# Performance work log

Measured on AMD Instinct MI355X. Metric: run time of the kernel, lower is better.

The kernel has to match this reference:

```python
import jax, jax.numpy as jnp
import numpy as np

B, S, T, D = 4, 512, 512, 256


def setup_inputs() -> dict:
    key = jax.random.key(0)
    ks = jax.random.split(key, 10)
    scale = 1.0 / np.sqrt(D)
    return {
        "source": jax.random.normal(ks[0], (B, S, D), jnp.float32),
        "target": jax.random.normal(ks[1], (B, T, D), jnp.float32),
        "W_src": jax.random.uniform(ks[2], (D, D), jnp.float32, -scale, scale),
        "b_src": jax.random.uniform(ks[3], (D,), jnp.float32, -scale, scale),
        "W_tgt": jax.random.uniform(ks[4], (D, D), jnp.float32, -scale, scale),
        "b_tgt": jax.random.uniform(ks[5], (D,), jnp.float32, -scale, scale),
        "W_res": jax.random.uniform(ks[6], (D, 1), jnp.float32, -scale, scale),
        "b_res": jax.random.uniform(ks[7], (1,), jnp.float32, -scale, scale),
        "W_prob": jax.random.uniform(ks[8], (D, 2), jnp.float32, -scale, scale),
        "b_prob": jax.random.uniform(ks[9], (2,), jnp.float32, -scale, scale),
    }


def reference(source, target, W_src, b_src, W_tgt, b_tgt, W_res, b_res, W_prob, b_prob):
    # source: (B,S,D), target: (B,T,D)
    src_lin = jnp.einsum("bsd,de->bse", source, W_src) + b_src  # (B,S,D)
    tgt_lin = jnp.einsum("btd,de->bte", target, W_tgt) + b_tgt  # (B,T,D)
    # Bahdanau-style additive attention: (B,T,S,D) broadcast, tanh, D->1
    h = jnp.tanh(src_lin[:, None, :, :] + tgt_lin[:, :, None, :])  # (B,T,S,D)
    genP = jnp.einsum("btsd,d->bts", h, W_res[:, 0]) + b_res[0]     # (B,T,S)
    prob = jax.nn.softmax(jnp.einsum("btd,de->bte", target, W_prob) + b_prob, axis=-1)  # (B,T,2)
    return genP, prob
```

## Files before the change

kernel.cpp:

```cpp
#include <hip/hip_runtime.h>

#define B_ 4
#define S_ 512
#define T_ 512
#define D_ 256
#define NSRC (B_ * S_)
#define K2F 2.8853900817779268f

typedef __attribute__((ext_vector_type(8))) short short8;
typedef __attribute__((ext_vector_type(4))) float f32x4;
typedef __attribute__((ext_vector_type(2))) float f32x2;

__device__ __forceinline__ unsigned short f2bf(float f) {
    union { float f; unsigned u; } v; v.f = f;
    unsigned r = v.u + 0x7FFF + ((v.u >> 16) & 1);
    return (unsigned short)(r >> 16);
}

__global__ __launch_bounds__(256) void prep_kernel(
    const float* __restrict__ src, const float* __restrict__ tgt,
    const float* __restrict__ Wsrc, const float* __restrict__ Wtgt,
    const float* __restrict__ Wp, const float* __restrict__ bp,
    unsigned short* __restrict__ abf, unsigned short* __restrict__ wtb,
    float* __restrict__ out)
{
    __shared__ float tl[64 * 65];
    const int blk = blockIdx.x, tid = threadIdx.x;

    if (blk < 1024) {
        int i4 = blk * 256 + tid;
        const int half = NSRC * D_ / 4;
        const float4* in = (i4 < half) ? (const float4*)src : (const float4*)tgt;
        int j = (i4 < half) ? i4 : i4 - half;
        float4 v = in[j];
        ushort4 o;
        o.x = f2bf(v.x); o.y = f2bf(v.y); o.z = f2bf(v.z); o.w = f2bf(v.w);
        *(ushort4*)&abf[i4 * 4] = o;
    } else if (blk < 1056) {
        int wb = blk - 1024;
        int e = wb >> 4, ti = wb & 15, tr = ti >> 2, tc = ti & 3;
        int r0 = tr * 64, c0 = tc * 64;
        const float* W = e ? Wtgt : Wsrc;
        #pragma unroll
        for (int it = 0; it < 4; it++) {
            int rr = (tid >> 4) + it * 16;
            int cc = (tid & 15) * 4;
            float4 v = *(const float4*)&W[(r0 + rr) * D_ + c0 + cc];
            tl[(cc + 0) * 65 + rr] = v.x;
            tl[(cc + 1) * 65 + rr] = v.y;
            tl[(cc + 2) * 65 + rr] = v.z;
            tl[(cc + 3) * 65 + rr] = v.w;
        }
        __syncthreads();
        #pragma unroll
        for (int it = 0; it < 2; it++) {
            int jj = (tid >> 3) + it * 32;
            int kk = (tid & 7) * 8;
            ushort4 lo, hi;
            lo.x = f2bf(tl[jj * 65 + kk + 0]); lo.y = f2bf(tl[jj * 65 + kk + 1]);
            lo.z = f2bf(tl[jj * 65 + kk + 2]); lo.w = f2bf(tl[jj * 65 + kk + 3]);
            hi.x = f2bf(tl[jj * 65 + kk + 4]); hi.y = f2bf(tl[jj * 65 + kk + 5]);
            hi.z = f2bf(tl[jj * 65 + kk + 6]); hi.w = f2bf(tl[jj * 65 + kk + 7]);
            int idx = (e * 256 + c0 + jj) * D_ + r0 + kk;
            *(ushort4*)&wtb[idx] = lo;
            *(ushort4*)&wtb[idx + 4] = hi;
        }
    } else {
        int row  = (blk - 1056) * 4 + (tid >> 6);
        int lane = tid & 63;
        float p0 = 0.f, p1 = 0.f;
        #pragma unroll
        for (int i = 0; i < 4; i++) {
            int d = lane + i * 64;
            float v = tgt[row * D_ + d];
            float2 w = *(const float2*)&Wp[d * 2];
            p0 = fmaf(v, w.x, p0);
            p1 = fmaf(v, w.y, p1);
        }
        #pragma unroll
        for (int off = 32; off > 0; off >>= 1) {
            p0 += __shfl_down(p0, off, 64);
            p1 += __shfl_down(p1, off, 64);
        }
        if (lane == 0) {
            const float L2E = 1.4426950408889634f;
            float l0 = p0 + bp[0], l1 = p1 + bp[1];
            float e10 = __builtin_amdgcn_exp2f((l1 - l0) * L2E);
            float e01 = __builtin_amdgcn_exp2f((l0 - l1) * L2E);
            out[B_ * T_ * S_ + row * 2 + 0] = __builtin_amdgcn_rcpf(1.f + e10);
            out[B_ * T_ * S_ + row * 2 + 1] = __builtin_amdgcn_rcpf(1.f + e01);
        }
    }
}

#define LSTR 68
__global__ __launch_bounds__(768, 1) void mega_kernel(
    const unsigned short* __restrict__ abf, const unsigned short* __restrict__ wtb,
    const float* __restrict__ bsrc, const float* __restrict__ btgt,
    const float* __restrict__ Wres, const float* __restrict__ bres,
    float* __restrict__ out)
{
    __shared__ float ls[2][64 * LSTR];
    __shared__ float lt[2][64 * LSTR];
    __shared__ float c0s;

    const int tid = threadIdx.x;
    const int lane = tid & 63, w = tid >> 6;
    const int s0 = blockIdx.x * 64;
    const int t0 = blockIdx.y * 64;
    const int b  = blockIdx.z;

    if (w == 0) {
        float s = Wres[lane] + Wres[lane + 64] + Wres[lane + 128] + Wres[lane + 192];
        #pragma unroll
        for (int off = 32; off > 0; off >>= 1) s += __shfl_xor(s, off, 64);
        if (lane == 0) c0s = s + bres[0];
    }

    const bool producer = (w < 4);

    const int pw  = w & 3;
    const int mat = pw >> 1;
    const int rb  = 2 * (pw & 1);
    const int n = lane & 15, quad = lane >> 4;
    const float* bias = mat ? btgt : bsrc;
    const unsigned short* wtbase = wtb + mat * 256 * D_;
    const int R0 = mat ? (NSRC + b * T_ + t0) : (b * S_ + s0);

    short8 af[2][8];
    if (producer) {
        #pragma unroll
        for (int rg = 0; rg < 2; rg++)
            #pragma unroll
            for (int ks = 0; ks < 8; ks++)
                af[rg][ks] = *(const short8*)&abf[(R0 + (rb + rg) * 16 + n) * D_ + ks * 32 + quad * 8];
    }

    auto phaseA = [&](int c, int bi) {
        float* lx = (mat ? lt[bi] : ls[bi]);
        #pragma unroll
        for (int cg = 0; cg < 4; cg++) {
            const int gcol = c * 4 + cg;
            const unsigned short* bptr = &wtbase[(gcol * 16 + n) * D_ + quad * 8];
            short8 bf[8];
            #pragma unroll
            for (int ks = 0; ks < 8; ks++) bf[ks] = *(const short8*)&bptr[ks * 32];
            const int dloc = cg * 16 + n;
            const float bv = bias[gcol * 16 + n];
            #pragma unroll
            for (int rg = 0; rg < 2; rg++) {
                f32x4 a4 = {0.f, 0.f, 0.f, 0.f};
                #pragma unroll
                for (int ks = 0; ks < 8; ks++)
                    a4 = __builtin_amdgcn_mfma_f32_16x16x32_bf16(af[rg][ks], bf[ks], a4, 0, 0, 0);
                float4 o;
                o.x = __builtin_amdgcn_exp2f((a4[0] + bv) * K2F);
                o.y = __builtin_amdgcn_exp2f((a4[1] + bv) * K2F);
                o.z = __builtin_amdgcn_exp2f((a4[2] + bv) * K2F);
                o.w = __builtin_amdgcn_exp2f((a4[3] + bv) * K2F);
                *(float4*)&lx[dloc * LSTR + (rb + rg) * 16 + quad * 4] = o;
            }
        }
    };

    const int cl = tid - 256;
    const int m = cl & 15;
    const int g = cl >> 4;
    f32x2 acc[2][2];
    #pragma unroll
    for (int i = 0; i < 2; i++) {
        acc[i][0] = (f32x2){0.f, 0.f};
        acc[i][1] = (f32x2){0.f, 0.f};
    }

    if (producer) phaseA(0, 0);
    __syncthreads();

    for (int c = 0; c < 4; c++) {
        const int bi = c & 1;
        if (producer) {
            if (c < 3) phaseA(c + 1, bi ^ 1);
        } else {
            const float* lsb = ls[bi];
            const float* ltb = lt[bi];
            const float* wp = &Wres[c * 64];
            const f32x2 one2 = {1.f, 1.f};
            #pragma unroll 8
            for (int kp = 0; kp < 32; kp++) {
                const int d0 = 2 * kp, d1 = 2 * kp + 1;
                float4 av0 = *(const float4*)&lsb[d0 * LSTR + 4 * m];
                float4 av1 = *(const float4*)&lsb[d1 * LSTR + 4 * m];
                float2 cv0 = *(const float2*)&ltb[d0 * LSTR + 2 * g];
                float2 cv1 = *(const float2*)&ltb[d1 * LSTR + 2 * g];
                const float w0 = wp[d0], w1 = wp[d1];
                const f32x2 w0v = {w0, w0}, w1v = {w1, w1};
                f32x2 a0p[2] = {{av0.x, av0.y}, {av0.z, av0.w}};
                f32x2 a1p[2] = {{av1.x, av1.y}, {av1.z, av1.w}};
                const float cc0[2] = {cv0.x, cv0.y};
                const float cc1[2] = {cv1.x, cv1.y};
                #pragma unroll
                for (int i = 0; i < 2; i++) {
                    const f32x2 c0v = {cc0[i], cc0[i]};
                    const f32x2 c1v = {cc1[i], cc1[i]};
                    #pragma unroll
                    for (int jp = 0; jp < 2; jp++) {
                        f32x2 dd0 = a0p[jp] * c0v + one2;
                        f32x2 dd1 = a1p[jp] * c1v + one2;
                        f32x2 den = dd0 * dd1;
                        f32x2 tnu = dd0 * w1v;
                        f32x2 num = dd1 * w0v + tnu;
                        f32x2 r;
                        r.x = __builtin_amdgcn_rcpf(den.x);
                        r.y = __builtin_amdgcn_rcpf(den.y);
                        acc[i][jp] = num * r + acc[i][jp];
                    }
                }
            }
        }
        __syncthreads();
    }

    if (!producer) {
        const float C0 = c0s;
        #pragma unroll
        for (int i = 0; i < 2; i++) {
            float4 o;
            o.x = C0 - 2.f * acc[i][0].x;
            o.y = C0 - 2.f * acc[i][0].y;
            o.z = C0 - 2.f * acc[i][1].x;
            o.w = C0 - 2.f * acc[i][1].y;
            *(float4*)&out[(b * T_ + t0 + 2 * g + i) * S_ + s0 + 4 * m] = o;
        }
    }
}

extern "C" void kernel_launch(void* const* d_in, const int* in_sizes, int n_in,
                              void* d_out, int out_size, void* d_ws, size_t ws_size,
                              hipStream_t stream) {
    const float* source = (const float*)d_in[0];
    const float* target = (const float*)d_in[1];
    const float* W_src  = (const float*)d_in[2];
    const float* b_src  = (const float*)d_in[3];
    const float* W_tgt  = (const float*)d_in[4];
    const float* b_tgt  = (const float*)d_in[5];
    const float* W_res  = (const float*)d_in[6];
    const float* b_res  = (const float*)d_in[7];
    const float* W_prob = (const float*)d_in[8];
    const float* b_prob = (const float*)d_in[9];
    float* out = (float*)d_out;

    unsigned short* abf = (unsigned short*)d_ws;
    unsigned short* wtb = abf + 2 * NSRC * D_;

    prep_kernel<<<1568, 256, 0, stream>>>(source, target, W_src, W_tgt,
                                          W_prob, b_prob, abf, wtb, out);
    mega_kernel<<<dim3(8, 8, 4), 768, 0, stream>>>(abf, wtb, b_src, b_tgt,
                                                   W_res, b_res, out);
}
```

Baseline: 110.8 us.

## Split fused projection into separate MFMA kernel and wider genP kernel

The fused producer/consumer kernel is split in two. A new kernel computes the exponentiated linear projections once with MFMA and writes them transposed to workspace. The genP kernel then loads tiles from global memory and uses all 16 waves for the tanh-sum, splitting the D dimension across four wave groups and reducing the partial sums through shared memory. This stops each block from recomputing the projections for its tile and raises the number of waves doing the main compute, at the cost of an extra launch, a global round trip for the projections, and extra synchronisation for the reduction.

```diff
diff --git a/kernel.cpp b/kernel.cpp
--- a/kernel.cpp
+++ b/kernel.cpp
@@ -93,15 +93,64 @@
     }
 }
 
-#define LSTR 68
-__global__ __launch_bounds__(768, 1) void mega_kernel(
+__global__ __launch_bounds__(256) void linT_kernel(
     const unsigned short* __restrict__ abf, const unsigned short* __restrict__ wtb,
     const float* __restrict__ bsrc, const float* __restrict__ btgt,
+    float* __restrict__ yaT, float* __restrict__ ycT)
+{
+    int wid  = blockIdx.x * 4 + (threadIdx.x >> 6);
+    int lane = threadIdx.x & 63;
+    int rg = wid >> 3;
+    int cg = wid & 7;
+    int e  = rg >> 7;
+    int r0 = rg * 16;
+    int n = lane & 15, quad = lane >> 4;
+
+    const float* bias = e ? btgt : bsrc;
+    float* outT = e ? ycT : yaT;
+    int orow0 = r0 - e * NSRC;
+
+    int ct0 = cg * 2, ct1 = cg * 2 + 1;
+    f32x4 acc0 = {0.f, 0.f, 0.f, 0.f};
+    f32x4 acc1 = {0.f, 0.f, 0.f, 0.f};
+
+    const unsigned short* aP  = &abf[(r0 + n) * D_ + quad * 8];
+    const unsigned short* b0P = &wtb[(e * 256 + ct0 * 16 + n) * D_ + quad * 8];
+    const unsigned short* b1P = &wtb[(e * 256 + ct1 * 16 + n) * D_ + quad * 8];
+
+    #pragma unroll
+    for (int ks = 0; ks < 8; ks++) {
+        short8 a  = *(const short8*)&aP[ks * 32];
+        short8 b0 = *(const short8*)&b0P[ks * 32];
+        short8 b1 = *(const short8*)&b1P[ks * 32];
+        acc0 = __builtin_amdgcn_mfma_f32_16x16x32_bf16(a, b0, acc0, 0, 0, 0);
+        acc1 = __builtin_amdgcn_mfma_f32_16x16x32_bf16(a, b1, acc1, 0, 0, 0);
+    }
+
+    float b0v = bias[ct0 * 16 + n];
+    float b1v = bias[ct1 * 16 + n];
+    float4 o0, o1;
+    o0.x = __builtin_amdgcn_exp2f((acc0[0] + b0v) * K2F);
+    o0.y = __builtin_amdgcn_exp2f((acc0[1] + b0v) * K2F);
+    o0.z = __builtin_amdgcn_exp2f((acc0[2] + b0v) * K2F);
+    o0.w = __builtin_amdgcn_exp2f((acc0[3] + b0v) * K2F);
+    o1.x = __builtin_amdgcn_exp2f((acc1[0] + b1v) * K2F);
+    o1.y = __builtin_amdgcn_exp2f((acc1[1] + b1v) * K2F);
+    o1.z = __builtin_amdgcn_exp2f((acc1[2] + b1v) * K2F);
+    o1.w = __builtin_amdgcn_exp2f((acc1[3] + b1v) * K2F);
+    *(float4*)&outT[(ct0 * 16 + n) * NSRC + orow0 + quad * 4] = o0;
+    *(float4*)&outT[(ct1 * 16 + n) * NSRC + orow0 + quad * 4] = o1;
+}
+
+#define GSTR 68
+__global__ __launch_bounds__(1024, 4) void genp_kernel(
+    const float* __restrict__ yaT, const float* __restrict__ ycT,
     const float* __restrict__ Wres, const float* __restrict__ bres,
     float* __restrict__ out)
 {
-    __shared__ float ls[2][64 * LSTR];
-    __shared__ float lt[2][64 * LSTR];
+    __shared__ float lbuf[2 * 64 * GSTR];
+    float* ls = lbuf;
+    float* lt = lbuf + 64 * GSTR;
     __shared__ float c0s;
 
     const int tid = threadIdx.x;
@@ -109,6 +158,8 @@
     const int s0 = blockIdx.x * 64;
     const int t0 = blockIdx.y * 64;
     const int b  = blockIdx.z;
+    const int sg = b * S_ + s0;
+    const int tg = b * T_ + t0;
 
     if (w == 0) {
         float s = Wres[lane] + Wres[lane + 64] + Wres[lane + 128] + Wres[lane + 192];
@@ -117,119 +168,102 @@
         if (lane == 0) c0s = s + bres[0];
     }
 
-    const bool producer = (w < 4);
-
-    const int pw  = w & 3;
-    const int mat = pw >> 1;
-    const int rb  = 2 * (pw & 1);
-    const int n = lane & 15, quad = lane >> 4;
-    const float* bias = mat ? btgt : bsrc;
-    const unsigned short* wtbase = wtb + mat * 256 * D_;
-    const int R0 = mat ? (NSRC + b * T_ + t0) : (b * S_ + s0);
-
-    short8 af[2][8];
-    if (producer) {
-        #pragma unroll
-        for (int rg = 0; rg < 2; rg++)
-            #pragma unroll
-            for (int ks = 0; ks < 8; ks++)
-                af[rg][ks] = *(const short8*)&abf[(R0 + (rb + rg) * 16 + n) * D_ + ks * 32 + quad * 8];
-    }
-
-    auto phaseA = [&](int c, int bi) {
-        float* lx = (mat ? lt[bi] : ls[bi]);
-        #pragma unroll
-        for (int cg = 0; cg < 4; cg++) {
-            const int gcol = c * 4 + cg;
-            const unsigned short* bptr = &wtbase[(gcol * 16 + n) * D_ + quad * 8];
-            short8 bf[8];
-            #pragma unroll
-            for (int ks = 0; ks < 8; ks++) bf[ks] = *(const short8*)&bptr[ks * 32];
-            const int dloc = cg * 16 + n;
-            const float bv = bias[gcol * 16 + n];
-            #pragma unroll
-            for (int rg = 0; rg < 2; rg++) {
-                f32x4 a4 = {0.f, 0.f, 0.f, 0.f};
-                #pragma unroll
-                for (int ks = 0; ks < 8; ks++)
-                    a4 = __builtin_amdgcn_mfma_f32_16x16x32_bf16(af[rg][ks], bf[ks], a4, 0, 0, 0);
-                float4 o;
-                o.x = __builtin_amdgcn_exp2f((a4[0] + bv) * K2F);
-                o.y = __builtin_amdgcn_exp2f((a4[1] + bv) * K2F);
-                o.z = __builtin_amdgcn_exp2f((a4[2] + bv) * K2F);
-                o.w = __builtin_amdgcn_exp2f((a4[3] + bv) * K2F);
-                *(float4*)&lx[dloc * LSTR + (rb + rg) * 16 + quad * 4] = o;
-            }
-        }
-    };
-
-    const int cl = tid - 256;
-    const int m = cl & 15;
-    const int g = cl >> 4;
-    f32x2 acc[2][2];
+    const int q = w >> 2;
+    const int m = lane & 15;
+    const int g = (w & 3) * 4 + (lane >> 4);
+    const int dbase = q * 16;
+
+    f32x2 acc[4][2];
     #pragma unroll
-    for (int i = 0; i < 2; i++) {
+    for (int i = 0; i < 4; i++) {
         acc[i][0] = (f32x2){0.f, 0.f};
         acc[i][1] = (f32x2){0.f, 0.f};
     }
 
-    if (producer) phaseA(0, 0);
-    __syncthreads();
-
     for (int c = 0; c < 4; c++) {
-        const int bi = c & 1;
-        if (producer) {
-            if (c < 3) phaseA(c + 1, bi ^ 1);
-        } else {
-            const float* lsb = ls[bi];
-            const float* ltb = lt[bi];
-            const float* wp = &Wres[c * 64];
-            const f32x2 one2 = {1.f, 1.f};
-            #pragma unroll 8
-            for (int kp = 0; kp < 32; kp++) {
-                const int d0 = 2 * kp, d1 = 2 * kp + 1;
-                float4 av0 = *(const float4*)&lsb[d0 * LSTR + 4 * m];
-                float4 av1 = *(const float4*)&lsb[d1 * LSTR + 4 * m];
-                float2 cv0 = *(const float2*)&ltb[d0 * LSTR + 2 * g];
-                float2 cv1 = *(const float2*)&ltb[d1 * LSTR + 2 * g];
-                const float w0 = wp[d0], w1 = wp[d1];
-                const f32x2 w0v = {w0, w0}, w1v = {w1, w1};
-                f32x2 a0p[2] = {{av0.x, av0.y}, {av0.z, av0.w}};
-                f32x2 a1p[2] = {{av1.x, av1.y}, {av1.z, av1.w}};
-                const float cc0[2] = {cv0.x, cv0.y};
-                const float cc1[2] = {cv1.x, cv1.y};
+        __syncthreads();
+        #pragma unroll
+        for (int j = 0; j < 8; j++) {
+            int r = w * 8 + j;
+            if (r < 64) ls[r * GSTR + lane] = yaT[(c * 64 + r) * NSRC + sg + lane];
+            else        lt[(r - 64) * GSTR + lane] = ycT[(c * 64 + r - 64) * NSRC + tg + lane];
+        }
+        __syncthreads();
+
+        const float* wp = &Wres[c * 64 + dbase];
+        const f32x2 one2 = {1.f, 1.f};
+        #pragma unroll
+        for (int kp = 0; kp < 8; kp++) {
+            const int d0 = dbase + 2 * kp, d1 = d0 + 1;
+            float4 av0 = *(const float4*)&ls[d0 * GSTR + 4 * m];
+            float4 av1 = *(const float4*)&ls[d1 * GSTR + 4 * m];
+            float4 cv0 = *(const float4*)&lt[d0 * GSTR + 4 * g];
+            float4 cv1 = *(const float4*)&lt[d1 * GSTR + 4 * g];
+            const float w0 = wp[2 * kp], w1 = wp[2 * kp + 1];
+            const f32x2 w0v = {w0, w0}, w1v = {w1, w1};
+            f32x2 a0p[2] = {{av0.x, av0.y}, {av0.z, av0.w}};
+            f32x2 a1p[2] = {{av1.x, av1.y}, {av1.z, av1.w}};
+            const float cc0[4] = {cv0.x, cv0.y, cv0.z, cv0.w};
+            const float cc1[4] = {cv1.x, cv1.y, cv1.z, cv1.w};
+            #pragma unroll
+            for (int i = 0; i < 4; i++) {
+                const f32x2 c0v = {cc0[i], cc0[i]};
+                const f32x2 c1v = {cc1[i], cc1[i]};
                 #pragma unroll
-                for (int i = 0; i < 2; i++) {
-                    const f32x2 c0v = {cc0[i], cc0[i]};
-                    const f32x2 c1v = {cc1[i], cc1[i]};
-                    #pragma unroll
-                    for (int jp = 0; jp < 2; jp++) {
-                        f32x2 dd0 = a0p[jp] * c0v + one2;
-                        f32x2 dd1 = a1p[jp] * c1v + one2;
-                        f32x2 den = dd0 * dd1;
-                        f32x2 tnu = dd0 * w1v;
-                        f32x2 num = dd1 * w0v + tnu;
-                        f32x2 r;
-                        r.x = __builtin_amdgcn_rcpf(den.x);
-                        r.y = __builtin_amdgcn_rcpf(den.y);
-                        acc[i][jp] = num * r + acc[i][jp];
-                    }
+                for (int jp = 0; jp < 2; jp++) {
+                    f32x2 dd0 = a0p[jp] * c0v + one2;
+                    f32x2 dd1 = a1p[jp] * c1v + one2;
+                    f32x2 den = dd0 * dd1;
+                    f32x2 tnu = dd0 * w1v;
+                    f32x2 num = dd1 * w0v + tnu;
+                    f32x2 r;
+                    r.x = __builtin_amdgcn_rcpf(den.x);
+                    r.y = __builtin_amdgcn_rcpf(den.y);
+                    acc[i][jp] = num * r + acc[i][jp];
                 }
             }
         }
-        __syncthreads();
-    }
-
-    if (!producer) {
+    }
+
+    __syncthreads();
+    const int slot = ((w & 3) * 64 + lane) * 17;
+    const int slotH = ((q >> 1) * 256 + (w & 3) * 64 + lane) * 17;
+    if (q == 1 || q == 3) {
+        #pragma unroll
+        for (int i = 0; i < 4; i++) {
+            float4 p = {acc[i][0].x, acc[i][0].y, acc[i][1].x, acc[i][1].y};
+            *(float4*)&lbuf[slotH + 4 * i] = p;
+        }
+    }
+    __syncthreads();
+    if (q == 0 || q == 2) {
+        #pragma unroll
+        for (int i = 0; i < 4; i++) {
+            float4 p = *(const float4*)&lbuf[slotH + 4 * i];
+            acc[i][0].x += p.x; acc[i][0].y += p.y;
+            acc[i][1].x += p.z; acc[i][1].y += p.w;
+        }
+    }
+    __syncthreads();
+    if (q == 2) {
+        #pragma unroll
+        for (int i = 0; i < 4; i++) {
+            float4 p = {acc[i][0].x, acc[i][0].y, acc[i][1].x, acc[i][1].y};
+            *(float4*)&lbuf[slot + 4 * i] = p;
+        }
+    }
+    __syncthreads();
+    if (q == 0) {
         const float C0 = c0s;
         #pragma unroll
-        for (int i = 0; i < 2; i++) {
+        for (int i = 0; i < 4; i++) {
+            float4 p = *(const float4*)&lbuf[slot + 4 * i];
             float4 o;
-            o.x = C0 - 2.f * acc[i][0].x;
-            o.y = C0 - 2.f * acc[i][0].y;
-            o.z = C0 - 2.f * acc[i][1].x;
-            o.w = C0 - 2.f * acc[i][1].y;
-            *(float4*)&out[(b * T_ + t0 + 2 * g + i) * S_ + s0 + 4 * m] = o;
+            o.x = C0 - 2.f * (acc[i][0].x + p.x);
+            o.y = C0 - 2.f * (acc[i][0].y + p.y);
+            o.z = C0 - 2.f * (acc[i][1].x + p.z);
+            o.w = C0 - 2.f * (acc[i][1].y + p.w);
+            *(float4*)&out[(b * T_ + t0 + 4 * g + i) * S_ + s0 + 4 * m] = o;
         }
     }
 }
@@ -251,9 +285,11 @@
 
     unsigned short* abf = (unsigned short*)d_ws;
     unsigned short* wtb = abf + 2 * NSRC * D_;
+    float* yaT = (float*)(wtb + 2 * D_ * D_);
+    float* ycT = yaT + D_ * NSRC;
 
     prep_kernel<<<1568, 256, 0, stream>>>(source, target, W_src, W_tgt,
                                           W_prob, b_prob, abf, wtb, out);
-    mega_kernel<<<dim3(8, 8, 4), 768, 0, stream>>>(abf, wtb, b_src, b_tgt,
-                                                   W_res, b_res, out);
-}
+    linT_kernel<<<512, 256, 0, stream>>>(abf, wtb, b_src, b_tgt, yaT, ycT);
+    genp_kernel<<<dim3(8, 8, 4), 1024, 0, stream>>>(yaT, ycT, W_res, b_res, out);
+}
```

Result: slower. 118.8 us (+7.2%).
